# Kernel optimization log

Measured on AMD Instinct MI355X. Metric: run time of the kernel, lower is better.

The kernel has to match this reference:

```python
import jax, jax.numpy as jnp
import numpy as np

EMB_DIM = 1024
N_HEADS = 16
HEAD_DIM = EMB_DIM // N_HEADS
B, T = 2, 2048


def setup_inputs() -> dict:
    key = jax.random.key(0)
    ks = jax.random.split(key, 5)
    scale = 1.0 / np.sqrt(EMB_DIM)
    x = jax.random.normal(ks[0], (B, T, EMB_DIM), dtype=jnp.float32)
    # causal mask: True means masked (as in torch masked_fill)
    mask = jnp.triu(jnp.ones((T, T), dtype=bool), k=1)[None, None, :, :]
    WQ = jax.random.normal(ks[1], (EMB_DIM, EMB_DIM), dtype=jnp.float32) * scale
    WK = jax.random.normal(ks[2], (EMB_DIM, EMB_DIM), dtype=jnp.float32) * scale
    WV = jax.random.normal(ks[3], (EMB_DIM, EMB_DIM), dtype=jnp.float32) * scale
    WO = jax.random.normal(ks[4], (EMB_DIM, EMB_DIM), dtype=jnp.float32) * scale
    return {"x": x, "mask": mask, "WQ": WQ, "WK": WK, "WV": WV, "WO": WO}


def reference(x, mask, WQ, WK, WV, WO):
    Bb, Tt, E = x.shape
    H, D = N_HEADS, HEAD_DIM

    def split(y):  # [B,T,E] -> [B,H,T,D]
        return y.reshape(Bb, Tt, H, D).transpose(0, 2, 1, 3)

    # nn.Linear(bias=False): y = x @ W.T with W of shape [out, in]
    Q = split(jnp.einsum('bte,oe->bto', x, WQ))
    K = split(jnp.einsum('bte,oe->bto', x, WK))
    V = split(jnp.einsum('bte,oe->bto', x, WV))

    scores = jnp.einsum('bhqd,bhkd->bhqk', Q, K) / jnp.sqrt(jnp.float32(D))
    scores = jnp.where(mask, -jnp.inf, scores)
    w = jax.nn.softmax(scores, axis=-1)
    w = jnp.nan_to_num(w, nan=0.0)  # fully-masked rows -> 0, as in torch
    out = jnp.einsum('bhqk,bhkd->bhqd', w, V)
    # dropout is identity at inference (eval mode)
    merged = out.transpose(0, 2, 1, 3).reshape(Bb, Tt, E)
    y = jnp.einsum('bte,oe->bto', merged, WO)
    return y, w
```

## Files before the change

kernel.cpp:

```cpp
#include <hip/hip_runtime.h>
#include <cstdint>
#include <cstddef>

typedef __attribute__((ext_vector_type(4))) float  f32x4;
typedef __attribute__((ext_vector_type(8))) short  s16x8;
typedef __attribute__((ext_vector_type(4))) short  s16x4;

#define EMB   1024
#define NHEAD 16
#define HD    64
#define NB    2
#define TT    2048
#define TQKV  3072

__device__ __forceinline__ short f2bf(float f) {
  union { float f; unsigned u; } x; x.f = f;
  unsigned r = x.u + 0x7FFFu + ((x.u >> 16) & 1u);
  return (short)(r >> 16);
}

__device__ __forceinline__ float bf2f(short h) {
  union { unsigned u; float f; } x;
  x.u = ((unsigned)(unsigned short)h) << 16;
  return x.f;
}

__device__ __forceinline__ void gload_lds16(const short* g, short* l) {
  __builtin_amdgcn_global_load_lds(
      (const __attribute__((address_space(1))) void*)(g),
      (__attribute__((address_space(3))) void*)(l), 16, 0, 0);
}

__device__ __forceinline__ void bar_vm0() {
  asm volatile("s_waitcnt vmcnt(0)" ::: "memory");
  __builtin_amdgcn_sched_barrier(0);
  __builtin_amdgcn_s_barrier();
  __builtin_amdgcn_sched_barrier(0);
}
__device__ __forceinline__ void bar_vm1() {
  asm volatile("s_waitcnt vmcnt(1)" ::: "memory");
  __builtin_amdgcn_sched_barrier(0);
  __builtin_amdgcn_s_barrier();
  __builtin_amdgcn_sched_barrier(0);
}
__device__ __forceinline__ void bar_vm4() {
  asm volatile("s_waitcnt vmcnt(4)" ::: "memory");
  __builtin_amdgcn_sched_barrier(0);
  __builtin_amdgcn_s_barrier();
  __builtin_amdgcn_sched_barrier(0);
}

__global__ __launch_bounds__(256) void cvt_all(
    const float* __restrict__ x,  const float* __restrict__ wq,
    const float* __restrict__ wk, const float* __restrict__ wv,
    const float* __restrict__ wo,
    short* __restrict__ xb, short* __restrict__ wqkv, short* __restrict__ wob) {
  int i = blockIdx.x * 256 + threadIdx.x;
  const float* s; short* d; int off;
  if (i < 1048576) { s = x; d = xb; off = i; }
  else {
    int j = i - 1048576;
    int r = j >> 18;
    off = j & 262143;
    s = (r == 0) ? wq : (r == 1) ? wk : (r == 2) ? wv : wo;
    d = (r == 3) ? wob : wqkv + (size_t)r * 1048576;
  }
  f32x4 v = ((const f32x4*)s)[off];
  s16x4 o;
  o[0] = f2bf(v[0]); o[1] = f2bf(v[1]); o[2] = f2bf(v[2]); o[3] = f2bf(v[3]);
  ((s16x4*)d)[off] = o;
}

template <int OUT_BF16>
__global__ __launch_bounds__(512) void gemm_nt(const short* __restrict__ A,
                                               const short* __restrict__ B,
                                               void* __restrict__ C,
                                               int M, int N, int K) {
  __shared__ short lA[2][128 * 32];
  __shared__ short lB[2][128 * 32];
  const int tid  = threadIdx.x;
  const int lane = tid & 63;
  const int wid  = tid >> 6;
  const int bm = blockIdx.y, bn = blockIdx.x;
  const int wm = wid >> 2, wn = wid & 3;

  f32x4 acc[4][2];
#pragma unroll
  for (int i = 0; i < 4; ++i)
#pragma unroll
    for (int j = 0; j < 2; ++j) acc[i][j] = (f32x4){0.f, 0.f, 0.f, 0.f};

  const short* Ab = A + (size_t)bm * 128 * K;
  const short* Bb = B + (size_t)bn * 128 * K;
  const int srow = tid >> 2;
  const int scol = (((tid & 3) ^ (srow & 3))) * 8;

#define G_STAGE(buf, k0)                                                     \
  do {                                                                       \
    gload_lds16(Ab + (size_t)srow * K + (k0) + scol, &lA[buf][tid * 8]);     \
    gload_lds16(Bb + (size_t)srow * K + (k0) + scol, &lB[buf][tid * 8]);     \
  } while (0)

  G_STAGE(0, 0);
  int cur = 0;
  for (int k0 = 0; k0 < K; k0 += 32) {
    __syncthreads();
    if (k0 + 32 < K) G_STAGE(cur ^ 1, k0 + 32);

    s16x8 af[4], bf_[2];
#pragma unroll
    for (int i = 0; i < 4; ++i) {
      const int ra = wm * 64 + i * 16 + (lane & 15);
      af[i] = *(const s16x8*)(&lA[cur][ra * 32 + (((lane >> 4) ^ (ra & 3)) << 3)]);
    }
#pragma unroll
    for (int j = 0; j < 2; ++j) {
      const int rb = wn * 32 + j * 16 + (lane & 15);
      bf_[j] = *(const s16x8*)(&lB[cur][rb * 32 + (((lane >> 4) ^ (rb & 3)) << 3)]);
    }
#pragma unroll
    for (int i = 0; i < 4; ++i)
#pragma unroll
      for (int j = 0; j < 2; ++j)
        acc[i][j] = __builtin_amdgcn_mfma_f32_16x16x32_bf16(af[i], bf_[j], acc[i][j], 0, 0, 0);
    cur ^= 1;
  }
#undef G_STAGE

  const int row0 = bm * 128 + wm * 64;
  const int col0 = bn * 128 + wn * 32;
#pragma unroll
  for (int i = 0; i < 4; ++i)
#pragma unroll
    for (int j = 0; j < 2; ++j)
#pragma unroll
      for (int r = 0; r < 4; ++r) {
        int row = row0 + i * 16 + ((lane >> 4) << 2) + r;
        int col = col0 + j * 16 + (lane & 15);
        float v = acc[i][j][r];
        if (OUT_BF16) ((short*)C)[(size_t)row * N + col] = f2bf(v);
        else          ((float*)C)[(size_t)row * N + col] = v;
      }
}

__global__ __launch_bounds__(256) void transpose_v(const short* __restrict__ qkv,
                                                   short* __restrict__ vt) {
  __shared__ short tile[64 * 72];
  const int tt = blockIdx.x, bh = blockIdx.y;
  const int b = bh >> 4, h = bh & 15;
  const int tid = threadIdx.x;

  const short* src = qkv + ((size_t)(b * TT + tt * 64)) * TQKV + 2048 + h * HD;
#pragma unroll
  for (int p = 0; p < 2; ++p) {
    int r = p * 32 + (tid >> 3);
    int c = (tid & 7) * 8;
    s16x8 v = *(const s16x8*)(src + (size_t)r * TQKV + c);
#pragma unroll
    for (int j = 0; j < 8; ++j) tile[r * 72 + c + j] = v[j];
  }
  __syncthreads();
  short* dst = vt + ((size_t)bh * HD) * TT + tt * 64;
#pragma unroll
  for (int p = 0; p < 2; ++p) {
    int d0 = p * 32 + (tid >> 3);
    int c  = (tid & 7) * 8;
    s16x8 o;
#pragma unroll
    for (int j = 0; j < 8; ++j) o[j] = tile[(c + j) * 72 + d0];
    *(s16x8*)(dst + (size_t)d0 * TT + c) = o;
  }
}

__global__ __launch_bounds__(512) void attn_fused(const short* __restrict__ qkv,
                                                  const short* __restrict__ vt,
                                                  float* __restrict__ wout,
                                                  short* __restrict__ merged) {
  __shared__ short smem[28672];
  short* const lW  = smem;
  short* const lK0 = smem + 8192;
  short* const lK1 = smem + 12288;
  short* const lK2 = smem + 16384;
  short* const lV0 = smem + 20480;
  short* const lV1 = smem + 24576;

  const int tid = threadIdx.x, lane = tid & 63, wid = tid >> 6;
  const int bh = blockIdx.y;
  const int qt = (blockIdx.y < 16) ? (15 - blockIdx.x) : blockIdx.x;
  const int b = bh >> 4, h = bh & 15;
  const int NT = 2 * qt + 2;

  const int srow = tid >> 3;
  const int scol = ((tid & 7) ^ (srow & 7)) * 8;
  const int frow = wid * 16 + (lane & 15);
  const int fcs  = (lane >> 4) * 8;
  const int qsub = (lane >> 4) << 2;
  const int qrow = qt * 128 + wid * 16 + qsub;

  const short* ksrc0 = qkv + (size_t)(b * TT) * TQKV + EMB + h * HD;
  const short* vsrc0 = vt + (size_t)bh * HD * TT;

#define STAGE_K(dst, kt)                                                       \
  gload_lds16(ksrc0 + (size_t)((kt) * 64 + srow) * TQKV + scol, (dst) + tid * 8)
#define STAGE_V(dst, kt)                                                       \
  gload_lds16(vsrc0 + (size_t)srow * TT + (kt) * 64 + scol,     (dst) + tid * 8)

  const short* qsrc = qkv + ((size_t)(b * TT + qt * 128)) * TQKV + h * HD;
  gload_lds16(qsrc + (size_t)srow * TQKV + scol,        lW + tid * 8);
  gload_lds16(qsrc + (size_t)(srow + 64) * TQKV + scol, lW + 4096 + tid * 8);
  __syncthreads();

  s16x8 aq[2];
  aq[0] = *(const s16x8*)(lW + frow * 64 + ((fcs)      ^ ((frow & 7) << 3)));
  aq[1] = *(const s16x8*)(lW + frow * 64 + ((32 + fcs) ^ ((frow & 7) << 3)));

  float l[4] = {0.f, 0.f, 0.f, 0.f};
  {
    short *p0 = lK0, *p1 = lK1, *p2 = lK2;
    STAGE_K(p0, 0);
    STAGE_K(p1, 1);
    bar_vm0();
    for (int kt = 0; kt < NT; ++kt) {
      const bool pre = (kt + 2 < NT);
      if (pre) STAGE_K(p2, kt + 2);

      f32x4 s[4];
#pragma unroll
      for (int nj = 0; nj < 4; ++nj) s[nj] = (f32x4){0.f, 0.f, 0.f, 0.f};
#pragma unroll
      for (int ks2 = 0; ks2 < 2; ++ks2)
#pragma unroll
        for (int nj = 0; nj < 4; ++nj) {
          int br = nj * 16 + (lane & 15);
          s16x8 bk = *(const s16x8*)(p0 + br * 64 + ((ks2 * 32 + fcs) ^ ((br & 7) << 3)));
          s[nj] = __builtin_amdgcn_mfma_f32_16x16x32_bf16(aq[ks2], bk, s[nj], 0, 0, 0);
        }

      const int kc = kt * 64 + (lane & 15);
#pragma unroll
      for (int r = 0; r < 4; ++r) {
        const int q = qrow + r;
#pragma unroll
        for (int nj = 0; nj < 4; ++nj)
          if (kc + nj * 16 <= q) l[r] += __expf(s[nj][r] * 0.125f);
      }

      if (pre) bar_vm1();
      else     bar_vm0();
      short* t_ = p0; p0 = p1; p1 = p2; p2 = t_;
    }
  }
  float rl[4];
#pragma unroll
  for (int r = 0; r < 4; ++r) {
    float e = l[r];
    e += __shfl_xor(e, 1);
    e += __shfl_xor(e, 2);
    e += __shfl_xor(e, 4);
    e += __shfl_xor(e, 8);
    rl[r] = 1.0f / e;
  }

  f32x4 o[4];
#pragma unroll
  for (int nj = 0; nj < 4; ++nj) o[nj] = (f32x4){0.f, 0.f, 0.f, 0.f};

  {
    short *kc_ = lK0, *kn_ = lK1, *vc_ = lV0, *vn_ = lV1;
    STAGE_K(kc_, 0);
    STAGE_V(vc_, 0);
    bar_vm0();
    for (int kt = 0; kt < NT; ++kt) {
      f32x4 s[4];
#pragma unroll
      for (int nj = 0; nj < 4; ++nj) s[nj] = (f32x4){0.f, 0.f, 0.f, 0.f};
#pragma unroll
      for (int ks2 = 0; ks2 < 2; ++ks2)
#pragma unroll
        for (int nj = 0; nj < 4; ++nj) {
          int br = nj * 16 + (lane & 15);
          s16x8 bk = *(const s16x8*)(kc_ + br * 64 + ((ks2 * 32 + fcs) ^ ((br & 7) << 3)));
          s[nj] = __builtin_amdgcn_mfma_f32_16x16x32_bf16(aq[ks2], bk, s[nj], 0, 0, 0);
        }

      const bool pre = (kt + 1 < NT);
      if (pre) { STAGE_K(kn_, kt + 1); STAGE_V(vn_, kt + 1); }
      __builtin_amdgcn_sched_barrier(0);

      const int kc = kt * 64 + (lane & 15);
#pragma unroll
      for (int r = 0; r < 4; ++r) {
        const int q = qrow + r;
        const int wrow = wid * 16 + qsub + r;
        const int sw = (wrow & 7) << 3;
#pragma unroll
        for (int nj = 0; nj < 4; ++nj) {
          const int col = nj * 16 + (lane & 15);
          float wv = (kc + nj * 16 <= q) ? __expf(s[nj][r] * 0.125f) * rl[r] : 0.f;
          lW[wrow * 64 + (col ^ sw)] = f2bf(wv);
        }
      }

      {
        const int zrow = wid * 16 + (lane >> 2);
        const int zc   = (lane & 3) * 16;
        const int sw2  = (zrow & 7) << 3;
        s16x8 h0 = *(const s16x8*)(lW + zrow * 64 + (zc ^ sw2));
        s16x8 h1 = *(const s16x8*)(lW + zrow * 64 + ((zc + 8) ^ sw2));
        f32x4 w0, w1, w2, w3;
#pragma unroll
        for (int k = 0; k < 4; ++k) {
          w0[k] = bf2f(h0[k]); w1[k] = bf2f(h0[k + 4]);
          w2[k] = bf2f(h1[k]); w3[k] = bf2f(h1[k + 4]);
        }
        float* wr = wout + ((size_t)bh * TT + qt * 128 + zrow) * TT + kt * 64 + zc;
        *(f32x4*)(wr)      = w0;
        *(f32x4*)(wr + 4)  = w1;
        *(f32x4*)(wr + 8)  = w2;
        *(f32x4*)(wr + 12) = w3;
      }

#pragma unroll
      for (int ks2 = 0; ks2 < 2; ++ks2) {
        s16x8 aw = *(const s16x8*)(lW + frow * 64 + ((ks2 * 32 + fcs) ^ ((frow & 7) << 3)));
#pragma unroll
        for (int nj = 0; nj < 4; ++nj) {
          int br = nj * 16 + (lane & 15);
          s16x8 bv = *(const s16x8*)(vc_ + br * 64 + ((ks2 * 32 + fcs) ^ ((br & 7) << 3)));
          o[nj] = __builtin_amdgcn_mfma_f32_16x16x32_bf16(aw, bv, o[nj], 0, 0, 0);
        }
      }

      if (pre) {
        bar_vm4();
        short* t_;
        t_ = kc_; kc_ = kn_; kn_ = t_;
        t_ = vc_; vc_ = vn_; vn_ = t_;
      }
    }
  }
#undef STAGE_K
#undef STAGE_V

#pragma unroll
  for (int nj = 0; nj < 4; ++nj)
#pragma unroll
    for (int r = 0; r < 4; ++r)
      merged[(size_t)(b * TT + qrow + r) * EMB + h * HD + nj * 16 + (lane & 15)] = f2bf(o[nj][r]);

  {
    const int zrow = tid >> 2, zc = (tid & 3) * 16;
    float* zbase = wout + ((size_t)bh * TT + qt * 128 + zrow) * TT + zc;
    const f32x4 z = (f32x4){0.f, 0.f, 0.f, 0.f};
    for (int kt = NT; kt < TT / 64; ++kt) {
      float* p = zbase + kt * 64;
      *(f32x4*)(p)      = z;
      *(f32x4*)(p + 4)  = z;
      *(f32x4*)(p + 8)  = z;
      *(f32x4*)(p + 12) = z;
    }
  }
}

extern "C" void kernel_launch(void* const* d_in, const int* in_sizes, int n_in,
                              void* d_out, int out_size, void* d_ws, size_t ws_size,
                              hipStream_t stream) {
  const float* x  = (const float*)d_in[0];
  const float* WQ = (const float*)d_in[2];
  const float* WK = (const float*)d_in[3];
  const float* WV = (const float*)d_in[4];
  const float* WO = (const float*)d_in[5];

  float* y    = (float*)d_out;
  float* wout = (float*)d_out + (size_t)NB * TT * EMB;

  char* ws = (char*)d_ws;
  short* xb     = (short*)(ws + 0);
  short* wqkv   = (short*)(ws + 8388608);
  short* wob    = (short*)(ws + 14680064);
  short* qkvb   = (short*)(ws + 16777216);
  short* vtb    = (short*)(ws + 41943040);
  short* merged = (short*)(ws + 50331648);

  cvt_all<<<8192, 256, 0, stream>>>(x, WQ, WK, WV, WO, xb, wqkv, wob);

  gemm_nt<1><<<dim3(24, 32), 512, 0, stream>>>(xb, wqkv, qkvb, 4096, 3072, 1024);

  transpose_v<<<dim3(32, 32), 256, 0, stream>>>(qkvb, vtb);

  attn_fused<<<dim3(16, 32), 512, 0, stream>>>(qkvb, vtb, wout, merged);

  gemm_nt<0><<<dim3(8, 32), 512, 0, stream>>>(merged, wob, y, 4096, 1024, 1024);
}
```

Before: 279.0 us.

## Transpose QK^T MFMA so each lane owns a query row; write fp32 weights directly

Swaps the MFMA operands for the score computation so each lane holds contiguous key columns for a single query row. This lets the full-precision softmax weights be stored to global memory straight from registers as f32x4, with no LDS round trip and bf16 re-expansion. Exponentials switch to exp2 with the log-sum folded in as an additive offset, masking is skipped for fully unmasked tiles, and bf16 packing uses v_cvt_pk_bf16_f32. Row-sum reduction shrinks to two shuffles. The stored weights now carry fp32 precision instead of bf16-rounded values, and global store coalescing shifts to a per-lane row pattern.

```diff
diff --git a/kernel.cpp b/kernel.cpp
--- a/kernel.cpp
+++ b/kernel.cpp
@@ -5,6 +5,7 @@
 typedef __attribute__((ext_vector_type(4))) float  f32x4;
 typedef __attribute__((ext_vector_type(8))) short  s16x8;
 typedef __attribute__((ext_vector_type(4))) short  s16x4;
+typedef __attribute__((ext_vector_type(2))) unsigned int u32x2;
 
 #define EMB   1024
 #define NHEAD 16
@@ -13,16 +14,18 @@
 #define TT    2048
 #define TQKV  3072
 
+#define C_EXP2 0.18033688011112042f
+
 __device__ __forceinline__ short f2bf(float f) {
   union { float f; unsigned u; } x; x.f = f;
   unsigned r = x.u + 0x7FFFu + ((x.u >> 16) & 1u);
   return (short)(r >> 16);
 }
 
-__device__ __forceinline__ float bf2f(short h) {
-  union { unsigned u; float f; } x;
-  x.u = ((unsigned)(unsigned short)h) << 16;
-  return x.f;
+__device__ __forceinline__ unsigned cvt_pk_bf16(float lo, float hi) {
+  unsigned r;
+  asm("v_cvt_pk_bf16_f32 %0, %1, %2" : "=v"(r) : "v"(lo), "v"(hi));
+  return r;
 }
 
 __device__ __forceinline__ void gload_lds16(const short* g, short* l) {
@@ -192,10 +195,15 @@
 
   const int srow = tid >> 3;
   const int scol = ((tid & 7) ^ (srow & 7)) * 8;
-  const int frow = wid * 16 + (lane & 15);
+  const int q15  = lane & 15;
   const int fcs  = (lane >> 4) * 8;
+  const int kg4  = (lane >> 4) << 2;
+  const int qg   = wid * 16 + q15;
+  const int qglob = qt * 128 + qg;
+  const int sw   = (q15 & 7) << 3;
   const int qsub = (lane >> 4) << 2;
   const int qrow = qt * 128 + wid * 16 + qsub;
+  const int wave_qmin = qt * 128 + wid * 16;
 
   const short* ksrc0 = qkv + (size_t)(b * TT) * TQKV + EMB + h * HD;
   const short* vsrc0 = vt + (size_t)bh * HD * TT;
@@ -211,10 +219,10 @@
   __syncthreads();
 
   s16x8 aq[2];
-  aq[0] = *(const s16x8*)(lW + frow * 64 + ((fcs)      ^ ((frow & 7) << 3)));
-  aq[1] = *(const s16x8*)(lW + frow * 64 + ((32 + fcs) ^ ((frow & 7) << 3)));
-
-  float l[4] = {0.f, 0.f, 0.f, 0.f};
+  aq[0] = *(const s16x8*)(lW + qg * 64 + ((fcs)      ^ ((qg & 7) << 3)));
+  aq[1] = *(const s16x8*)(lW + qg * 64 + ((32 + fcs) ^ ((qg & 7) << 3)));
+
+  float lsum = 0.f;
   {
     short *p0 = lK0, *p1 = lK1, *p2 = lK2;
     STAGE_K(p0, 0);
@@ -224,42 +232,36 @@
       const bool pre = (kt + 2 < NT);
       if (pre) STAGE_K(p2, kt + 2);
 
-      f32x4 s[4];
-#pragma unroll
-      for (int nj = 0; nj < 4; ++nj) s[nj] = (f32x4){0.f, 0.f, 0.f, 0.f};
+      f32x4 s2[4];
+#pragma unroll
+      for (int kg = 0; kg < 4; ++kg) s2[kg] = (f32x4){0.f, 0.f, 0.f, 0.f};
 #pragma unroll
       for (int ks2 = 0; ks2 < 2; ++ks2)
 #pragma unroll
-        for (int nj = 0; nj < 4; ++nj) {
-          int br = nj * 16 + (lane & 15);
-          s16x8 bk = *(const s16x8*)(p0 + br * 64 + ((ks2 * 32 + fcs) ^ ((br & 7) << 3)));
-          s[nj] = __builtin_amdgcn_mfma_f32_16x16x32_bf16(aq[ks2], bk, s[nj], 0, 0, 0);
-        }
-
-      const int kc = kt * 64 + (lane & 15);
-#pragma unroll
-      for (int r = 0; r < 4; ++r) {
-        const int q = qrow + r;
-#pragma unroll
-        for (int nj = 0; nj < 4; ++nj)
-          if (kc + nj * 16 <= q) l[r] += __expf(s[nj][r] * 0.125f);
-      }
+        for (int kg = 0; kg < 4; ++kg) {
+          s16x8 bk = *(const s16x8*)(p0 + (kg * 16 + q15) * 64 + ((ks2 * 32 + fcs) ^ sw));
+          s2[kg] = __builtin_amdgcn_mfma_f32_16x16x32_bf16(bk, aq[ks2], s2[kg], 0, 0, 0);
+        }
+
+      const bool full = (kt * 64 + 63 <= wave_qmin);
+      const int kb0 = kt * 64 + kg4;
+#pragma unroll
+      for (int kg = 0; kg < 4; ++kg)
+#pragma unroll
+        for (int r = 0; r < 4; ++r) {
+          float e = exp2f(s2[kg][r] * C_EXP2);
+          if (!full) e = (kb0 + kg * 16 + r <= qglob) ? e : 0.f;
+          lsum += e;
+        }
 
       if (pre) bar_vm1();
       else     bar_vm0();
       short* t_ = p0; p0 = p1; p1 = p2; p2 = t_;
     }
   }
-  float rl[4];
-#pragma unroll
-  for (int r = 0; r < 4; ++r) {
-    float e = l[r];
-    e += __shfl_xor(e, 1);
-    e += __shfl_xor(e, 2);
-    e += __shfl_xor(e, 4);
-    e += __shfl_xor(e, 8);
-    rl[r] = 1.0f / e;
-  }
+  lsum += __shfl_xor(lsum, 16);
+  lsum += __shfl_xor(lsum, 32);
+  const float lrl = -log2f(lsum);
 
   f32x4 o[4];
 #pragma unroll
@@ -270,63 +272,48 @@
     STAGE_K(kc_, 0);
     STAGE_V(vc_, 0);
     bar_vm0();
+    float* const wq_base = wout + ((size_t)bh * TT + qglob) * TT;
     for (int kt = 0; kt < NT; ++kt) {
-      f32x4 s[4];
-#pragma unroll
-      for (int nj = 0; nj < 4; ++nj) s[nj] = (f32x4){0.f, 0.f, 0.f, 0.f};
+      f32x4 s2[4];
+#pragma unroll
+      for (int kg = 0; kg < 4; ++kg) s2[kg] = (f32x4){0.f, 0.f, 0.f, 0.f};
 #pragma unroll
       for (int ks2 = 0; ks2 < 2; ++ks2)
 #pragma unroll
-        for (int nj = 0; nj < 4; ++nj) {
-          int br = nj * 16 + (lane & 15);
-          s16x8 bk = *(const s16x8*)(kc_ + br * 64 + ((ks2 * 32 + fcs) ^ ((br & 7) << 3)));
-          s[nj] = __builtin_amdgcn_mfma_f32_16x16x32_bf16(aq[ks2], bk, s[nj], 0, 0, 0);
+        for (int kg = 0; kg < 4; ++kg) {
+          s16x8 bk = *(const s16x8*)(kc_ + (kg * 16 + q15) * 64 + ((ks2 * 32 + fcs) ^ sw));
+          s2[kg] = __builtin_amdgcn_mfma_f32_16x16x32_bf16(bk, aq[ks2], s2[kg], 0, 0, 0);
         }
 
       const bool pre = (kt + 1 < NT);
       if (pre) { STAGE_K(kn_, kt + 1); STAGE_V(vn_, kt + 1); }
       __builtin_amdgcn_sched_barrier(0);
 
-      const int kc = kt * 64 + (lane & 15);
-#pragma unroll
-      for (int r = 0; r < 4; ++r) {
-        const int q = qrow + r;
-        const int wrow = wid * 16 + qsub + r;
-        const int sw = (wrow & 7) << 3;
+      const bool full = (kt * 64 + 63 <= wave_qmin);
+      float* wbase = wq_base + kt * 64 + kg4;
+#pragma unroll
+      for (int kg = 0; kg < 4; ++kg) {
+        f32x4 w4;
+#pragma unroll
+        for (int r = 0; r < 4; ++r) {
+          float e = exp2f(fmaf(s2[kg][r], C_EXP2, lrl));
+          w4[r] = (full || (kt * 64 + kg * 16 + kg4 + r <= qglob)) ? e : 0.f;
+        }
+        *(f32x4*)(wbase + kg * 16) = w4;
+        u32x2 pk2;
+        pk2.x = cvt_pk_bf16(w4[0], w4[1]);
+        pk2.y = cvt_pk_bf16(w4[2], w4[3]);
+        const int col = kg * 16 + kg4;
+        *(u32x2*)(lW + qg * 64 + (col ^ sw)) = pk2;
+      }
+      __builtin_amdgcn_sched_barrier(0);
+
+#pragma unroll
+      for (int ks2 = 0; ks2 < 2; ++ks2) {
+        s16x8 aw = *(const s16x8*)(lW + qg * 64 + ((ks2 * 32 + fcs) ^ ((qg & 7) << 3)));
 #pragma unroll
         for (int nj = 0; nj < 4; ++nj) {
-          const int col = nj * 16 + (lane & 15);
-          float wv = (kc + nj * 16 <= q) ? __expf(s[nj][r] * 0.125f) * rl[r] : 0.f;
-          lW[wrow * 64 + (col ^ sw)] = f2bf(wv);
-        }
-      }
-
-      {
-        const int zrow = wid * 16 + (lane >> 2);
-        const int zc   = (lane & 3) * 16;
-        const int sw2  = (zrow & 7) << 3;
-        s16x8 h0 = *(const s16x8*)(lW + zrow * 64 + (zc ^ sw2));
-        s16x8 h1 = *(const s16x8*)(lW + zrow * 64 + ((zc + 8) ^ sw2));
-        f32x4 w0, w1, w2, w3;
-#pragma unroll
-        for (int k = 0; k < 4; ++k) {
-          w0[k] = bf2f(h0[k]); w1[k] = bf2f(h0[k + 4]);
-          w2[k] = bf2f(h1[k]); w3[k] = bf2f(h1[k + 4]);
-        }
-        float* wr = wout + ((size_t)bh * TT + qt * 128 + zrow) * TT + kt * 64 + zc;
-        *(f32x4*)(wr)      = w0;
-        *(f32x4*)(wr + 4)  = w1;
-        *(f32x4*)(wr + 8)  = w2;
-        *(f32x4*)(wr + 12) = w3;
-      }
-
-#pragma unroll
-      for (int ks2 = 0; ks2 < 2; ++ks2) {
-        s16x8 aw = *(const s16x8*)(lW + frow * 64 + ((ks2 * 32 + fcs) ^ ((frow & 7) << 3)));
-#pragma unroll
-        for (int nj = 0; nj < 4; ++nj) {
-          int br = nj * 16 + (lane & 15);
-          s16x8 bv = *(const s16x8*)(vc_ + br * 64 + ((ks2 * 32 + fcs) ^ ((br & 7) << 3)));
+          s16x8 bv = *(const s16x8*)(vc_ + (nj * 16 + q15) * 64 + ((ks2 * 32 + fcs) ^ sw));
           o[nj] = __builtin_amdgcn_mfma_f32_16x16x32_bf16(aw, bv, o[nj], 0, 0, 0);
         }
       }
@@ -346,7 +333,7 @@
   for (int nj = 0; nj < 4; ++nj)
 #pragma unroll
     for (int r = 0; r < 4; ++r)
-      merged[(size_t)(b * TT + qrow + r) * EMB + h * HD + nj * 16 + (lane & 15)] = f2bf(o[nj][r]);
+      merged[(size_t)(b * TT + qrow + r) * EMB + h * HD + nj * 16 + q15] = f2bf(o[nj][r]);
 
   {
     const int zrow = tid >> 2, zc = (tid & 3) * 16;
```

Result: faster. 241.3 us (-13.5%).
